# Kernel optimization log

Measured on AMD Instinct MI355X. Metric: run time of the kernel, lower is better.

Reference implementation:

```python
import jax, jax.numpy as jnp
import numpy as np

B, S, D = 4, 2048, 512
QKD = 256
HID = 3 * D  # expansion_factor=3
EPS = 1e-5


def _ln(x, g, b):
    m = jnp.mean(x, axis=-1, keepdims=True)
    v = jnp.mean((x - m) ** 2, axis=-1, keepdims=True)
    return (x - m) * jax.lax.rsqrt(v + EPS) * g + b


def setup_inputs() -> dict:
    key = jax.random.key(0)
    ks = jax.random.split(key, 12)
    s = lambda fan: 1.0 / np.sqrt(fan)
    return {
        "x":  jax.random.normal(ks[0], (B, S, D), jnp.float32),
        "Wm": jax.random.uniform(ks[1], (D, D), jnp.float32, -s(D), s(D)),
        "bm": jnp.zeros((D,), jnp.float32),
        "g1": jnp.ones((D,), jnp.float32),
        "b1": jnp.zeros((D,), jnp.float32),
        "Wh": jax.random.uniform(ks[2], (2 * HID, D), jnp.float32, -s(D), s(D)),
        "bh": jnp.zeros((2 * HID,), jnp.float32),
        "Wq": jax.random.uniform(ks[3], (QKD, D), jnp.float32, -s(D), s(D)),
        "bq": jnp.zeros((QKD,), jnp.float32),
        "Wb": jax.random.normal(ks[4], (QKD, QKD), jnp.float32),
        "Wo": jax.random.uniform(ks[5], (D, HID), jnp.float32, -s(HID), s(HID)),
        "bo": jnp.zeros((D,), jnp.float32),
        "g2": jnp.ones((D,), jnp.float32),
        "b2": jnp.zeros((D,), jnp.float32),
    }


def reference(x, Wm, bm, g1, b1, Wh, bh, Wq, bq, Wb, Wo, bo, g2, b2):
    seq_len = x.shape[-2]
    memory = jnp.einsum('bsd,ed->bse', x, Wm) + bm
    normed = _ln(x + memory, g1, b1)
    h = jax.nn.relu(jnp.einsum('bsd,hd->bsh', normed, Wh) + bh)
    v, gate = h[..., :HID], h[..., HID:]
    Z = jax.nn.relu(jnp.einsum('bsd,qd->bsq', normed, Wq) + bq)  # [B,S,QKD]
    QK = jnp.einsum('bid,de,bje->bij', Z, Wb, Z) / seq_len
    A = jax.nn.relu(QK) ** 2  # relu^2 attention, no softmax
    V = jnp.einsum('bij,bjd->bid', A, v) * gate
    out = _ln(jnp.einsum('bsh,dh->bsd', V, Wo) + bo, g2, b2)
    return out + x
```

## Files before the change

kernel.cpp:

```cpp
#include <hip/hip_runtime.h>

typedef unsigned short u16;
typedef unsigned char u8;
typedef __attribute__((ext_vector_type(8))) short short8;
typedef __attribute__((ext_vector_type(4))) float f32x4;
typedef __attribute__((ext_vector_type(8))) int int8v;
typedef __attribute__((ext_vector_type(4))) int int4v;

#define LN_EPS 1e-5f
#define SCALE_A 4096.f
#define SCALE_V 8.f
#define INV_SCALE_AV (1.f/32768.f)
#define SCALE_NRM 4.f
#define SCALE_WH 512.f
#define INV_SCALE_H (1.f/2048.f)
#define MX_ONE 0x7F7F7F7Fu

__device__ __forceinline__ u16 f2bf(float f){
    union { float f; unsigned u; } c; c.f = f;
    unsigned u = c.u + 0x7FFFu + ((c.u >> 16) & 1u);
    return (u16)(u >> 16);
}
__device__ __forceinline__ float bf2f(u16 h){
    union { unsigned u; float f; } c; c.u = ((unsigned)h) << 16;
    return c.f;
}
__device__ __forceinline__ u8 f2fp8(float f){
    int r = __builtin_amdgcn_cvt_pk_fp8_f32(f, 0.f, 0, false);
    return (u8)(r & 0xFF);
}
__device__ __forceinline__ u16 f2fp8x2(float a, float b){
    int r = __builtin_amdgcn_cvt_pk_fp8_f32(a, b, 0, false);
    return (u16)(r & 0xFFFF);
}

enum { EPI_NONE=0, EPI_BIAS_RES, EPI_BIAS_RELU, EPI_RELUSQ };
enum { OT_F32=0, OT_BF16=1, OT_FP8=2 };

__device__ __forceinline__ void gl2lds16(const void* g, void* lds){
    __builtin_amdgcn_global_load_lds(
        (const __attribute__((address_space(1))) unsigned*)g,
        (__attribute__((address_space(3))) unsigned*)lds, 16, 0, 0);
}

template<int EPI, int OT>
__device__ __forceinline__ void bf16_gemm_body(
    u16* sA, u16* sB,
    const u16* Az, const u16* Bz, void* Cv,
    int K, int lda, int ldb, int ldc, size_t zc,
    int m0, int n0,
    const float* bias, const float* ext, int ldext, float scale)
{
    const int tid = threadIdx.x;
    const int lane = tid & 63, quad = lane >> 4, l15 = lane & 15;
    const int wave = tid >> 6;
    const int wm = (wave >> 1) * 64, wn = (wave & 1) * 64;

    const u16* gA[2]; const u16* gB[2]; int lo[2];
#pragma unroll
    for (int r = 0; r < 2; r++){
        const int c = tid + r * 256;
        gA[r] = Az + (size_t)(m0 + (c & 127)) * lda + (c >> 7) * 8;
        gB[r] = Bz + (size_t)(n0 + (c & 127)) * ldb + (c >> 7) * 8;
        lo[r] = ((tid & 192) + r * 256) * 16;
    }

    f32x4 acc[4][4];
#pragma unroll
    for (int i = 0; i < 4; i++)
#pragma unroll
        for (int j = 0; j < 4; j++) acc[i][j] = (f32x4){0.f,0.f,0.f,0.f};

    const u16* fA = sA + quad * 1024 + (wm + l15) * 8;
    const u16* fB = sB + quad * 1024 + (wn + l15) * 8;

    for (int k0 = 0; k0 < K; k0 += 32){
#pragma unroll
        for (int r = 0; r < 2; r++){
            gl2lds16(gA[r] + k0, (char*)sA + lo[r]);
            gl2lds16(gB[r] + k0, (char*)sB + lo[r]);
        }
        __syncthreads();
        short8 a[4], b[4];
#pragma unroll
        for (int t = 0; t < 4; t++){
            a[t] = *(const short8*)(fA + t * 128);
            b[t] = *(const short8*)(fB + t * 128);
        }
#pragma unroll
        for (int i = 0; i < 4; i++)
#pragma unroll
            for (int j = 0; j < 4; j++)
                acc[i][j] = __builtin_amdgcn_mfma_f32_16x16x32_bf16(a[i], b[j], acc[i][j], 0, 0, 0);
        __syncthreads();
    }

    float* Cf = (float*)Cv; u16* Ch = (u16*)Cv; u8* C8 = (u8*)Cv;
#pragma unroll
    for (int i = 0; i < 4; i++){
#pragma unroll
        for (int j = 0; j < 4; j++){
            const int n = n0 + wn + j * 16 + l15;
            float bs = (EPI==EPI_BIAS_RES || EPI==EPI_BIAS_RELU) ? bias[n] : 0.f;
#pragma unroll
            for (int r = 0; r < 4; r++){
                const int m = m0 + wm + i * 16 + quad * 4 + r;
                float v = acc[i][j][r] + bs;
                if (EPI==EPI_BIAS_RES) v += ext[(size_t)m * ldext + n];
                if (EPI==EPI_BIAS_RELU) v = fmaxf(v, 0.f);
                if (EPI==EPI_RELUSQ){ float t = fmaxf(v * scale, 0.f); v = t * t * SCALE_A; }
                if (OT==OT_FP8)       C8[zc + (size_t)m * ldc + n] = f2fp8(v);
                else if (OT==OT_BF16) Ch[zc + (size_t)m * ldc + n] = f2bf(v);
                else                  Cf[zc + (size_t)m * ldc + n] = v;
            }
        }
    }
}

template<int EPI, int OT>
__global__ __launch_bounds__(256)
void mgemm(const u16* __restrict__ A, const u16* __restrict__ B, void* __restrict__ Cv,
           int K, int lda, int ldb, int ldc,
           long sAb, long sBb, long sCb,
           const float* __restrict__ bias,
           const float* __restrict__ ext, int ldext,
           float scale)
{
    __shared__ u16 sA[4096];
    __shared__ u16 sB[4096];
    const int z = blockIdx.z;
    bf16_gemm_body<EPI,OT>(sA, sB,
        A + (size_t)z * sAb, B + (size_t)z * sBb, Cv,
        K, lda, ldb, ldc, (size_t)z * sCb,
        blockIdx.y * 128, blockIdx.x * 128,
        bias, ext, ldext, scale);
}

template<bool VOUT>
__device__ __forceinline__ void mx_gemm_body(
    u8* sA, u8* sB,
    const u8* Az, const u8* Bz, u16* C,
    int K, int lda, int ldb, int ldc, size_t zc,
    int m0, int n0,
    const u16* gate, int ldext, size_t ze,
    const float* bias, u8* vout)
{
    const int tid = threadIdx.x;
    const int lane = tid & 63, quad = lane >> 4, l15 = lane & 15;
    const int wave = tid >> 6;
    const int wm = (wave >> 1) * 64, wn = (wave & 1) * 64;

    const u8* gA[4]; const u8* gB[4]; int lo[4];
#pragma unroll
    for (int p = 0; p < 4; p++){
        const int r = p * 32 + (tid >> 3);
        const int j = (tid & 7) ^ (r & 7);
        gA[p] = Az + (size_t)(m0 + r) * lda + j * 16;
        gB[p] = Bz + (size_t)(n0 + r) * ldb + j * 16;
        lo[p] = p * 4096 + wave * 1024;
    }

    f32x4 acc[4][4];
#pragma unroll
    for (int i = 0; i < 4; i++)
#pragma unroll
        for (int j = 0; j < 4; j++) acc[i][j] = (f32x4){0.f,0.f,0.f,0.f};

    for (int k0 = 0; k0 < K; k0 += 128){
#pragma unroll
        for (int p = 0; p < 4; p++){
            gl2lds16(gA[p] + k0, (char*)sA + lo[p]);
            gl2lds16(gB[p] + k0, (char*)sB + lo[p]);
        }
        __syncthreads();
        int8v a[4], b[4];
#pragma unroll
        for (int i = 0; i < 4; i++){
            const int m = wm + i * 16 + l15;
            const int4v a0 = *(const int4v*)(sA + m * 128 + ((2*quad    ) ^ (m & 7)) * 16);
            const int4v a1 = *(const int4v*)(sA + m * 128 + ((2*quad + 1) ^ (m & 7)) * 16);
            a[i] = (int8v){a0[0],a0[1],a0[2],a0[3],a1[0],a1[1],a1[2],a1[3]};
            const int n = wn + i * 16 + l15;
            const int4v b0 = *(const int4v*)(sB + n * 128 + ((2*quad    ) ^ (n & 7)) * 16);
            const int4v b1 = *(const int4v*)(sB + n * 128 + ((2*quad + 1) ^ (n & 7)) * 16);
            b[i] = (int8v){b0[0],b0[1],b0[2],b0[3],b1[0],b1[1],b1[2],b1[3]};
        }
#pragma unroll
        for (int i = 0; i < 4; i++)
#pragma unroll
            for (int j = 0; j < 4; j++)
                acc[i][j] = __builtin_amdgcn_mfma_scale_f32_16x16x128_f8f6f4(
                    a[i], b[j], acc[i][j], 0, 0, 0, MX_ONE, 0, MX_ONE);
        __syncthreads();
    }

#pragma unroll
    for (int i = 0; i < 4; i++){
#pragma unroll
        for (int j = 0; j < 4; j++){
            const int n = n0 + wn + j * 16 + l15;
#pragma unroll
            for (int r = 0; r < 4; r++){
                const int m = m0 + wm + i * 16 + quad * 4 + r;
                if (VOUT){
                    float h = fmaxf(acc[i][j][r] * INV_SCALE_H + bias[n], 0.f);
                    vout[(size_t)m * 1536 + n] = f2fp8(h * SCALE_V);
                } else {
                    float v = acc[i][j][r] * INV_SCALE_AV
                            * bf2f(gate[ze + (size_t)m * ldext + n]);
                    C[zc + (size_t)m * ldc + n] = f2bf(v);
                }
            }
        }
    }
}

__global__ __launch_bounds__(256)
void mgemm8mx(const u8* __restrict__ A, const u8* __restrict__ B, u16* __restrict__ C,
              int K, int lda, int ldb, int ldc,
              long sAb, long sBb, long sCb,
              const u16* __restrict__ gate, int ldext, long sEb)
{
    __shared__ u8 sA[16384];
    __shared__ u8 sB[16384];
    const int z = blockIdx.z;
    mx_gemm_body<false>(sA, sB,
        A + (size_t)z * sAb, B + (size_t)z * sBb, C,
        K, lda, ldb, ldc, (size_t)z * sCb,
        blockIdx.y * 128, blockIdx.x * 128,
        gate, ldext, (size_t)z * sEb, nullptr, nullptr);
}

__global__ __launch_bounds__(256)
void dual3_k(const u16* __restrict__ nrm, const u16* __restrict__ n8,
             const u8* __restrict__ Wh8, const u16* __restrict__ Whgb,
             const u16* __restrict__ Wqbf,
             const float* __restrict__ bh, const float* __restrict__ bq,
             u8* __restrict__ v8, u16* __restrict__ gbf, u16* __restrict__ Zb)
{
    __shared__ char lds[32768];
    const int bx = blockIdx.x;
    const int m0 = blockIdx.y * 128;
    if (bx < 12){
        mx_gemm_body<true>((u8*)lds, (u8*)lds + 16384,
            (const u8*)n8, Wh8, nullptr,
            512, 512, 512, 0, 0,
            m0, bx * 128,
            nullptr, 0, 0, bh, v8);
    } else if (bx < 24){
        bf16_gemm_body<EPI_BIAS_RELU,OT_BF16>((u16*)lds, (u16*)lds + 4096,
            nrm, Whgb, gbf,
            512, 512, 512, 1536, 0,
            m0, (bx - 12) * 128,
            bh + 1536, nullptr, 0, 1.f);
    } else {
        bf16_gemm_body<EPI_BIAS_RELU,OT_BF16>((u16*)lds, (u16*)lds + 4096,
            nrm, Wqbf, Zb,
            512, 512, 512, 256, 0,
            m0, (bx - 24) * 128,
            bq, nullptr, 0, 1.f);
    }
}

__global__ __launch_bounds__(256)
void batch6_k(const u16* __restrict__ ZWbb, const u16* __restrict__ Zb,
              u8* __restrict__ A8,
              const u8* __restrict__ v8, u8* __restrict__ vT8)
{
    __shared__ char lds[16384];
    const int bx = blockIdx.x;
    const int z  = blockIdx.y;
    const int S = 2048, QKD = 256, HID = 1536;
    if (bx < 256){
        bf16_gemm_body<EPI_RELUSQ,OT_FP8>((u16*)lds, (u16*)lds + 4096,
            ZWbb + (size_t)z * S * QKD, Zb + (size_t)z * S * QKD, A8,
            QKD, QKD, QKD, S, (size_t)z * S * S,
            (bx >> 4) * 128, (bx & 15) * 128,
            nullptr, nullptr, 0, 1.f/(float)S);
    } else {
        const int idx = bx - 256;
        const int h0 = (idx % 24) * 64, s0 = (idx / 24) * 64;
        u8 (*t)[68] = (u8(*)[68])lds;
        const u8* vb = v8 + (size_t)z * S * HID;
        u8* vTb = vT8 + (size_t)z * HID * S;
        const int tid = threadIdx.x;
#pragma unroll
        for (int i = 0; i < 4; i++){
            int id2 = tid + i * 256;
            int r = id2 >> 4, c4 = (id2 & 15) * 4;
            uchar4 u = *(const uchar4*)(vb + (size_t)(s0 + r) * HID + h0 + c4);
            t[r][c4] = u.x; t[r][c4+1] = u.y; t[r][c4+2] = u.z; t[r][c4+3] = u.w;
        }
        __syncthreads();
#pragma unroll
        for (int i = 0; i < 4; i++){
            int id2 = tid + i * 256;
            int r = id2 >> 4, c4 = (id2 & 15) * 4;
            uchar4 u;
            u.x = t[c4][r]; u.y = t[c4+1][r]; u.z = t[c4+2][r]; u.w = t[c4+3][r];
            *(uchar4*)(vTb + (size_t)(h0 + r) * S + s0 + c4) = u;
        }
    }
}

__global__ __launch_bounds__(256)
void ln1_k(const float* __restrict__ in, const float* __restrict__ g,
           const float* __restrict__ b, u16* __restrict__ nbf, u16* __restrict__ n8)
{
    const int row = blockIdx.x, tid = threadIdx.x;
    const size_t base = (size_t)row * 512 + tid * 2;
    const float2 v = *(const float2*)(in + base);
    float s = v.x + v.y, ss = v.x * v.x + v.y * v.y;
#pragma unroll
    for (int off = 32; off > 0; off >>= 1){
        s  += __shfl_down(s,  off);
        ss += __shfl_down(ss, off);
    }
    __shared__ float sbuf[8], ssbuf[8];
    const int wid = tid >> 6, lane = tid & 63;
    if (lane == 0){ sbuf[wid] = s; ssbuf[wid] = ss; }
    __syncthreads();
    if (tid == 0){
        float S = 0.f, SS = 0.f;
#pragma unroll
        for (int i = 0; i < 4; i++){ S += sbuf[i]; SS += ssbuf[i]; }
        const float mean = S * (1.f/512.f);
        const float var  = SS * (1.f/512.f) - mean * mean;
        sbuf[4]  = mean;
        ssbuf[4] = rsqrtf(var + LN_EPS);
    }
    __syncthreads();
    const float mean = sbuf[4], rstd = ssbuf[4];
    const float2 gg = *(const float2*)(g + tid * 2);
    const float2 bb = *(const float2*)(b + tid * 2);
    const float ox = (v.x - mean) * rstd * gg.x + bb.x;
    const float oy = (v.y - mean) * rstd * gg.y + bb.y;
    ((unsigned*)nbf)[(size_t)row * 256 + tid] =
        ((unsigned)f2bf(oy) << 16) | (unsigned)f2bf(ox);
    n8[(size_t)row * 256 + tid] = f2fp8x2(ox * SCALE_NRM, oy * SCALE_NRM);
}

__global__ __launch_bounds__(256)
void ln2_k(const u16* __restrict__ pa, long pstride,
           const float* __restrict__ bias2,
           const float* __restrict__ g, const float* __restrict__ b,
           const float* __restrict__ x, float* __restrict__ out)
{
    const int row = blockIdx.x, tid = threadIdx.x;
    const size_t base = (size_t)row * 512 + tid * 2;
    const unsigned p0 = ((const unsigned*)pa)[(size_t)row * 256 + tid];
    const unsigned p1 = ((const unsigned*)(pa + pstride))[(size_t)row * 256 + tid];
    const float2 bb2 = *(const float2*)(bias2 + tid * 2);
    float2 v;
    v.x = bf2f((u16)p0) + bf2f((u16)p1) + bb2.x;
    v.y = bf2f((u16)(p0 >> 16)) + bf2f((u16)(p1 >> 16)) + bb2.y;
    float s = v.x + v.y, ss = v.x * v.x + v.y * v.y;
#pragma unroll
    for (int off = 32; off > 0; off >>= 1){
        s  += __shfl_down(s,  off);
        ss += __shfl_down(ss, off);
    }
    __shared__ float sbuf[8], ssbuf[8];
    const int wid = tid >> 6, lane = tid & 63;
    if (lane == 0){ sbuf[wid] = s; ssbuf[wid] = ss; }
    __syncthreads();
    if (tid == 0){
        float S = 0.f, SS = 0.f;
#pragma unroll
        for (int i = 0; i < 4; i++){ S += sbuf[i]; SS += ssbuf[i]; }
        const float mean = S * (1.f/512.f);
        const float var  = SS * (1.f/512.f) - mean * mean;
        sbuf[4]  = mean;
        ssbuf[4] = rsqrtf(var + LN_EPS);
    }
    __syncthreads();
    const float mean = sbuf[4], rstd = ssbuf[4];
    const float2 gg = *(const float2*)(g + tid * 2);
    const float2 bb = *(const float2*)(b + tid * 2);
    const float2 r = *(const float2*)(x + base);
    float2 o;
    o.x = (v.x - mean) * rstd * gg.x + bb.x + r.x;
    o.y = (v.y - mean) * rstd * gg.y + bb.y + r.y;
    *(float2*)(out + base) = o;
}

__global__ __launch_bounds__(256)
void castall_k(const float* __restrict__ x, const float* __restrict__ Wm,
               const float* __restrict__ Wh, const float* __restrict__ Wq,
               const float* __restrict__ Wo, const float* __restrict__ Wb,
               u16* __restrict__ xb, u16* __restrict__ Wmb, u8* __restrict__ Wh8,
               u16* __restrict__ Whgb,
               u16* __restrict__ Wqb, u16* __restrict__ Wob, u16* __restrict__ WbT)
{
    const int i = blockIdx.x * 256 + threadIdx.x;
    if (i >= 1736704){
        const int j = i - 1736704;
        if (j < 65536){
            const int e = j >> 8, d = j & 255;
            WbT[e * 256 + d] = f2bf(Wb[d * 256 + e]);
        }
        return;
    }
    if (i >= 1114112 && i < 1310720){
        const int off = i - 1114112;
        const float4 v = ((const float4*)Wh)[off];
        unsigned r0 = (unsigned)f2fp8x2(v.x * SCALE_WH, v.y * SCALE_WH);
        unsigned r1 = (unsigned)f2fp8x2(v.z * SCALE_WH, v.w * SCALE_WH);
        ((unsigned*)Wh8)[off] = r0 | (r1 << 16);
        return;
    }
    const float* src; u16* dst; int off;
    if      (i < 1048576){ src = x;  dst = xb;   off = i; }
    else if (i < 1114112){ src = Wm; dst = Wmb;  off = i - 1048576; }
    else if (i < 1507328){ src = Wh + 786432; dst = Whgb; off = i - 1310720; }
    else if (i < 1540096){ src = Wq; dst = Wqb;  off = i - 1507328; }
    else                 { src = Wo; dst = Wob;  off = i - 1540096; }
    const float4 v = ((const float4*)src)[off];
    ushort4 o; o.x = f2bf(v.x); o.y = f2bf(v.y); o.z = f2bf(v.z); o.w = f2bf(v.w);
    ((ushort4*)dst)[off] = o;
}

extern "C" void kernel_launch(void* const* d_in, const int* in_sizes, int n_in,
                              void* d_out, int out_size, void* d_ws, size_t ws_size,
                              hipStream_t stream)
{
    const float* x  = (const float*)d_in[0];
    const float* Wm = (const float*)d_in[1];
    const float* bm = (const float*)d_in[2];
    const float* g1 = (const float*)d_in[3];
    const float* b1 = (const float*)d_in[4];
    const float* Wh = (const float*)d_in[5];
    const float* bh = (const float*)d_in[6];
    const float* Wq = (const float*)d_in[7];
    const float* bq = (const float*)d_in[8];
    const float* Wb = (const float*)d_in[9];
    const float* Wo = (const float*)d_in[10];
    const float* bo = (const float*)d_in[11];
    const float* g2 = (const float*)d_in[12];
    const float* b2 = (const float*)d_in[13];
    float* out = (float*)d_out;
    (void)in_sizes; (void)n_in; (void)out_size; (void)ws_size;

    const int Bn=4, S=2048, D=512, QKD=256, HID=1536;
    const int M = Bn * S;
    const long MD = (long)M * D;

    char* p = (char*)d_ws;
    auto alloc = [&](size_t bytes)->void*{ void* r = p; p += (bytes + 255) & ~(size_t)255; return r; };
    u16*  xbf  = (u16*) alloc((size_t)M*D*2);
    u16*  Wmbf = (u16*) alloc((size_t)D*D*2);
    u8*   Wh8  = (u8*)  alloc((size_t)HID*D);
    u16*  Whgb = (u16*) alloc((size_t)HID*D*2);
    u16*  Wqbf = (u16*) alloc((size_t)QKD*D*2);
    u16*  Wobf = (u16*) alloc((size_t)D*HID*2);
    u16*  WbT  = (u16*) alloc((size_t)QKD*QKD*2);
    float* ybuf= (float*)alloc((size_t)MD*4);
    u16*  wop  = (u16*) alloc((size_t)MD*2*2);
    u16*  n8   = (u16*) alloc((size_t)M*D);
    u16*  Zb   = (u16*) alloc((size_t)M*QKD*2);
    u16*  ZWbb = (u16*) alloc((size_t)M*QKD*2);
    u8*   v8   = (u8*)  alloc((size_t)M*HID);
    u16*  gbf  = (u16*) alloc((size_t)M*HID*2);
    u8*   vT8  = (u8*)  alloc((size_t)M*HID);
    u8*   A8   = (u8*)  alloc((size_t)M*S);
    u16*  Vgbf = (u16*) alloc((size_t)M*HID*2);
    u16*  nrm  = xbf;

    dim3 blk(256);

    castall_k<<<dim3(7040), blk, 0, stream>>>(x, Wm, Wh, Wq, Wo, Wb,
                                              xbf, Wmbf, Wh8, Whgb, Wqbf, Wobf, WbT);
    mgemm<EPI_BIAS_RES,OT_F32><<<dim3(D/128, M/128, 1), blk, 0, stream>>>(
        xbf, Wmbf, ybuf, D, D, D, D, 0,0,0, bm, x, D, 1.f);
    ln1_k<<<dim3(M), blk, 0, stream>>>(ybuf, g1, b1, nrm, n8);
    dual3_k<<<dim3(26, M/128), blk, 0, stream>>>(
        nrm, n8, Wh8, Whgb, Wqbf, bh, bq, v8, gbf, Zb);
    mgemm<EPI_NONE,OT_BF16><<<dim3(QKD/128, M/128, 1), blk, 0, stream>>>(
        Zb, WbT, ZWbb, QKD, QKD, QKD, QKD, 0,0,0, nullptr, nullptr, 0, 1.f);
    batch6_k<<<dim3(1024, Bn), blk, 0, stream>>>(ZWbb, Zb, A8, v8, vT8);
    mgemm8mx<<<dim3(HID/128, S/128, Bn), blk, 0, stream>>>(
        A8, vT8, Vgbf, S, S, S, HID,
        (long)S*S, (long)HID*S, (long)S*HID,
        gbf, HID, (long)S*HID);
    mgemm<EPI_NONE,OT_BF16><<<dim3(D/128, M/128, 2), blk, 0, stream>>>(
        Vgbf, Wobf, wop, HID/2, HID, HID, D, 768, 768, MD,
        nullptr, nullptr, 0, 1.f);
    ln2_k<<<dim3(M), blk, 0, stream>>>(wop, MD, bo, g2, b2, x, out);
}
```

Before: 321.1 us.

## Fuse all stages into one persistent cooperative kernel with grid syncs

Replaces the nine separate kernel launches with a single cooperative persistent kernel. Each stage becomes a grid-stride loop over tiles or rows, and grid.sync() separates the stages. This removes per-launch overhead and the tail idle time between launches. In exchange it caps occupancy through a fixed grid size and launch bounds, gives every stage the larger 32KB LDS footprint, and adds grid-wide barrier cost and possible load imbalance.

```diff
diff --git a/kernel.cpp b/kernel.cpp
--- a/kernel.cpp
+++ b/kernel.cpp
@@ -1,4 +1,7 @@
 #include <hip/hip_runtime.h>
+#include <hip/hip_cooperative_groups.h>
+
+namespace cg = cooperative_groups;
 
 typedef unsigned short u16;
 typedef unsigned char u8;
@@ -115,25 +118,6 @@
             }
         }
     }
-}
-
-template<int EPI, int OT>
-__global__ __launch_bounds__(256)
-void mgemm(const u16* __restrict__ A, const u16* __restrict__ B, void* __restrict__ Cv,
-           int K, int lda, int ldb, int ldc,
-           long sAb, long sBb, long sCb,
-           const float* __restrict__ bias,
-           const float* __restrict__ ext, int ldext,
-           float scale)
-{
-    __shared__ u16 sA[4096];
-    __shared__ u16 sB[4096];
-    const int z = blockIdx.z;
-    bf16_gemm_body<EPI,OT>(sA, sB,
-        A + (size_t)z * sAb, B + (size_t)z * sBb, Cv,
-        K, lda, ldb, ldc, (size_t)z * sCb,
-        blockIdx.y * 128, blockIdx.x * 128,
-        bias, ext, ldext, scale);
 }
 
 template<bool VOUT>
@@ -215,235 +199,227 @@
     }
 }
 
-__global__ __launch_bounds__(256)
-void mgemm8mx(const u8* __restrict__ A, const u8* __restrict__ B, u16* __restrict__ C,
-              int K, int lda, int ldb, int ldc,
-              long sAb, long sBb, long sCb,
-              const u16* __restrict__ gate, int ldext, long sEb)
-{
-    __shared__ u8 sA[16384];
-    __shared__ u8 sB[16384];
-    const int z = blockIdx.z;
-    mx_gemm_body<false>(sA, sB,
-        A + (size_t)z * sAb, B + (size_t)z * sBb, C,
-        K, lda, ldb, ldc, (size_t)z * sCb,
-        blockIdx.y * 128, blockIdx.x * 128,
-        gate, ldext, (size_t)z * sEb, nullptr, nullptr);
-}
-
-__global__ __launch_bounds__(256)
-void dual3_k(const u16* __restrict__ nrm, const u16* __restrict__ n8,
-             const u8* __restrict__ Wh8, const u16* __restrict__ Whgb,
-             const u16* __restrict__ Wqbf,
-             const float* __restrict__ bh, const float* __restrict__ bq,
-             u8* __restrict__ v8, u16* __restrict__ gbf, u16* __restrict__ Zb)
-{
-    __shared__ char lds[32768];
-    const int bx = blockIdx.x;
-    const int m0 = blockIdx.y * 128;
-    if (bx < 12){
-        mx_gemm_body<true>((u8*)lds, (u8*)lds + 16384,
-            (const u8*)n8, Wh8, nullptr,
-            512, 512, 512, 0, 0,
-            m0, bx * 128,
-            nullptr, 0, 0, bh, v8);
-    } else if (bx < 24){
-        bf16_gemm_body<EPI_BIAS_RELU,OT_BF16>((u16*)lds, (u16*)lds + 4096,
-            nrm, Whgb, gbf,
-            512, 512, 512, 1536, 0,
-            m0, (bx - 12) * 128,
-            bh + 1536, nullptr, 0, 1.f);
-    } else {
-        bf16_gemm_body<EPI_BIAS_RELU,OT_BF16>((u16*)lds, (u16*)lds + 4096,
-            nrm, Wqbf, Zb,
-            512, 512, 512, 256, 0,
-            m0, (bx - 24) * 128,
-            bq, nullptr, 0, 1.f);
-    }
-}
-
-__global__ __launch_bounds__(256)
-void batch6_k(const u16* __restrict__ ZWbb, const u16* __restrict__ Zb,
-              u8* __restrict__ A8,
-              const u8* __restrict__ v8, u8* __restrict__ vT8)
-{
-    __shared__ char lds[16384];
-    const int bx = blockIdx.x;
-    const int z  = blockIdx.y;
-    const int S = 2048, QKD = 256, HID = 1536;
-    if (bx < 256){
-        bf16_gemm_body<EPI_RELUSQ,OT_FP8>((u16*)lds, (u16*)lds + 4096,
-            ZWbb + (size_t)z * S * QKD, Zb + (size_t)z * S * QKD, A8,
-            QKD, QKD, QKD, S, (size_t)z * S * S,
-            (bx >> 4) * 128, (bx & 15) * 128,
-            nullptr, nullptr, 0, 1.f/(float)S);
-    } else {
-        const int idx = bx - 256;
-        const int h0 = (idx % 24) * 64, s0 = (idx / 24) * 64;
-        u8 (*t)[68] = (u8(*)[68])lds;
-        const u8* vb = v8 + (size_t)z * S * HID;
-        u8* vTb = vT8 + (size_t)z * HID * S;
-        const int tid = threadIdx.x;
-#pragma unroll
-        for (int i = 0; i < 4; i++){
-            int id2 = tid + i * 256;
-            int r = id2 >> 4, c4 = (id2 & 15) * 4;
-            uchar4 u = *(const uchar4*)(vb + (size_t)(s0 + r) * HID + h0 + c4);
-            t[r][c4] = u.x; t[r][c4+1] = u.y; t[r][c4+2] = u.z; t[r][c4+3] = u.w;
-        }
-        __syncthreads();
-#pragma unroll
-        for (int i = 0; i < 4; i++){
-            int id2 = tid + i * 256;
-            int r = id2 >> 4, c4 = (id2 & 15) * 4;
-            uchar4 u;
-            u.x = t[c4][r]; u.y = t[c4+1][r]; u.z = t[c4+2][r]; u.w = t[c4+3][r];
-            *(uchar4*)(vTb + (size_t)(h0 + r) * S + s0 + c4) = u;
-        }
-    }
-}
-
-__global__ __launch_bounds__(256)
-void ln1_k(const float* __restrict__ in, const float* __restrict__ g,
-           const float* __restrict__ b, u16* __restrict__ nbf, u16* __restrict__ n8)
-{
-    const int row = blockIdx.x, tid = threadIdx.x;
-    const size_t base = (size_t)row * 512 + tid * 2;
-    const float2 v = *(const float2*)(in + base);
-    float s = v.x + v.y, ss = v.x * v.x + v.y * v.y;
-#pragma unroll
-    for (int off = 32; off > 0; off >>= 1){
-        s  += __shfl_down(s,  off);
-        ss += __shfl_down(ss, off);
-    }
-    __shared__ float sbuf[8], ssbuf[8];
-    const int wid = tid >> 6, lane = tid & 63;
-    if (lane == 0){ sbuf[wid] = s; ssbuf[wid] = ss; }
-    __syncthreads();
-    if (tid == 0){
-        float S = 0.f, SS = 0.f;
-#pragma unroll
-        for (int i = 0; i < 4; i++){ S += sbuf[i]; SS += ssbuf[i]; }
-        const float mean = S * (1.f/512.f);
-        const float var  = SS * (1.f/512.f) - mean * mean;
-        sbuf[4]  = mean;
-        ssbuf[4] = rsqrtf(var + LN_EPS);
-    }
-    __syncthreads();
-    const float mean = sbuf[4], rstd = ssbuf[4];
-    const float2 gg = *(const float2*)(g + tid * 2);
-    const float2 bb = *(const float2*)(b + tid * 2);
-    const float ox = (v.x - mean) * rstd * gg.x + bb.x;
-    const float oy = (v.y - mean) * rstd * gg.y + bb.y;
-    ((unsigned*)nbf)[(size_t)row * 256 + tid] =
-        ((unsigned)f2bf(oy) << 16) | (unsigned)f2bf(ox);
-    n8[(size_t)row * 256 + tid] = f2fp8x2(ox * SCALE_NRM, oy * SCALE_NRM);
-}
-
-__global__ __launch_bounds__(256)
-void ln2_k(const u16* __restrict__ pa, long pstride,
-           const float* __restrict__ bias2,
-           const float* __restrict__ g, const float* __restrict__ b,
-           const float* __restrict__ x, float* __restrict__ out)
-{
-    const int row = blockIdx.x, tid = threadIdx.x;
-    const size_t base = (size_t)row * 512 + tid * 2;
-    const unsigned p0 = ((const unsigned*)pa)[(size_t)row * 256 + tid];
-    const unsigned p1 = ((const unsigned*)(pa + pstride))[(size_t)row * 256 + tid];
-    const float2 bb2 = *(const float2*)(bias2 + tid * 2);
-    float2 v;
-    v.x = bf2f((u16)p0) + bf2f((u16)p1) + bb2.x;
-    v.y = bf2f((u16)(p0 >> 16)) + bf2f((u16)(p1 >> 16)) + bb2.y;
-    float s = v.x + v.y, ss = v.x * v.x + v.y * v.y;
-#pragma unroll
-    for (int off = 32; off > 0; off >>= 1){
-        s  += __shfl_down(s,  off);
-        ss += __shfl_down(ss, off);
-    }
-    __shared__ float sbuf[8], ssbuf[8];
-    const int wid = tid >> 6, lane = tid & 63;
-    if (lane == 0){ sbuf[wid] = s; ssbuf[wid] = ss; }
-    __syncthreads();
-    if (tid == 0){
-        float S = 0.f, SS = 0.f;
-#pragma unroll
-        for (int i = 0; i < 4; i++){ S += sbuf[i]; SS += ssbuf[i]; }
-        const float mean = S * (1.f/512.f);
-        const float var  = SS * (1.f/512.f) - mean * mean;
-        sbuf[4]  = mean;
-        ssbuf[4] = rsqrtf(var + LN_EPS);
-    }
-    __syncthreads();
-    const float mean = sbuf[4], rstd = ssbuf[4];
-    const float2 gg = *(const float2*)(g + tid * 2);
-    const float2 bb = *(const float2*)(b + tid * 2);
-    const float2 r = *(const float2*)(x + base);
-    float2 o;
-    o.x = (v.x - mean) * rstd * gg.x + bb.x + r.x;
-    o.y = (v.y - mean) * rstd * gg.y + bb.y + r.y;
-    *(float2*)(out + base) = o;
-}
-
-__global__ __launch_bounds__(256)
-void castall_k(const float* __restrict__ x, const float* __restrict__ Wm,
-               const float* __restrict__ Wh, const float* __restrict__ Wq,
-               const float* __restrict__ Wo, const float* __restrict__ Wb,
-               u16* __restrict__ xb, u16* __restrict__ Wmb, u8* __restrict__ Wh8,
-               u16* __restrict__ Whgb,
-               u16* __restrict__ Wqb, u16* __restrict__ Wob, u16* __restrict__ WbT)
-{
-    const int i = blockIdx.x * 256 + threadIdx.x;
+struct MegaArgs {
+    const float *x, *Wm, *bm, *g1, *b1, *Wh, *bh, *Wq, *bq, *Wb, *Wo, *bo, *g2, *b2;
+    float* out;
+    u16 *xbf, *Wmbf; u8* Wh8; u16 *Whgb, *Wqbf, *Wobf, *WbT;
+    float* ybuf; u16* wop; u16* n8; u16 *Zb, *ZWbb;
+    u8* v8; u16* gbf; u8 *vT8, *A8; u16* Vgbf;
+};
+
+__device__ __forceinline__ void cast_item(int i, const MegaArgs& a){
     if (i >= 1736704){
         const int j = i - 1736704;
         if (j < 65536){
             const int e = j >> 8, d = j & 255;
-            WbT[e * 256 + d] = f2bf(Wb[d * 256 + e]);
+            a.WbT[e * 256 + d] = f2bf(a.Wb[d * 256 + e]);
         }
         return;
     }
     if (i >= 1114112 && i < 1310720){
         const int off = i - 1114112;
-        const float4 v = ((const float4*)Wh)[off];
+        const float4 v = ((const float4*)a.Wh)[off];
         unsigned r0 = (unsigned)f2fp8x2(v.x * SCALE_WH, v.y * SCALE_WH);
         unsigned r1 = (unsigned)f2fp8x2(v.z * SCALE_WH, v.w * SCALE_WH);
-        ((unsigned*)Wh8)[off] = r0 | (r1 << 16);
+        ((unsigned*)a.Wh8)[off] = r0 | (r1 << 16);
         return;
     }
     const float* src; u16* dst; int off;
-    if      (i < 1048576){ src = x;  dst = xb;   off = i; }
-    else if (i < 1114112){ src = Wm; dst = Wmb;  off = i - 1048576; }
-    else if (i < 1507328){ src = Wh + 786432; dst = Whgb; off = i - 1310720; }
-    else if (i < 1540096){ src = Wq; dst = Wqb;  off = i - 1507328; }
-    else                 { src = Wo; dst = Wob;  off = i - 1540096; }
+    if      (i < 1048576){ src = a.x;  dst = a.xbf;   off = i; }
+    else if (i < 1114112){ src = a.Wm; dst = a.Wmbf;  off = i - 1048576; }
+    else if (i < 1507328){ src = a.Wh + 786432; dst = a.Whgb; off = i - 1310720; }
+    else if (i < 1540096){ src = a.Wq; dst = a.Wqbf;  off = i - 1507328; }
+    else                 { src = a.Wo; dst = a.Wobf;  off = i - 1540096; }
     const float4 v = ((const float4*)src)[off];
     ushort4 o; o.x = f2bf(v.x); o.y = f2bf(v.y); o.z = f2bf(v.z); o.w = f2bf(v.w);
     ((ushort4*)dst)[off] = o;
+}
+
+__device__ __forceinline__ void tr8_item(int z, int idx, const MegaArgs& a, char* lds){
+    const int S = 2048, HID = 1536;
+    const int h0 = (idx % 24) * 64, s0 = (idx / 24) * 64;
+    u8 (*t)[68] = (u8(*)[68])lds;
+    const u8* vb = a.v8 + (size_t)z * S * HID;
+    u8* vTb = a.vT8 + (size_t)z * HID * S;
+    const int tid = threadIdx.x;
+#pragma unroll
+    for (int i = 0; i < 4; i++){
+        int id2 = tid + i * 256;
+        int r = id2 >> 4, c4 = (id2 & 15) * 4;
+        uchar4 u = *(const uchar4*)(vb + (size_t)(s0 + r) * HID + h0 + c4);
+        t[r][c4] = u.x; t[r][c4+1] = u.y; t[r][c4+2] = u.z; t[r][c4+3] = u.w;
+    }
+    __syncthreads();
+#pragma unroll
+    for (int i = 0; i < 4; i++){
+        int id2 = tid + i * 256;
+        int r = id2 >> 4, c4 = (id2 & 15) * 4;
+        uchar4 u;
+        u.x = t[c4][r]; u.y = t[c4+1][r]; u.z = t[c4+2][r]; u.w = t[c4+3][r];
+        *(uchar4*)(vTb + (size_t)(h0 + r) * S + s0 + c4) = u;
+    }
+    __syncthreads();
+}
+
+__device__ __forceinline__ void ln_reduce(float2 v, float* sred, float& mean, float& rstd){
+    const int tid = threadIdx.x;
+    float s = v.x + v.y, ss = v.x * v.x + v.y * v.y;
+#pragma unroll
+    for (int off = 32; off > 0; off >>= 1){
+        s  += __shfl_down(s,  off);
+        ss += __shfl_down(ss, off);
+    }
+    float* sbuf = sred; float* ssbuf = sred + 8;
+    const int wid = tid >> 6, lane = tid & 63;
+    if (lane == 0){ sbuf[wid] = s; ssbuf[wid] = ss; }
+    __syncthreads();
+    if (tid == 0){
+        float S = 0.f, SS = 0.f;
+#pragma unroll
+        for (int i = 0; i < 4; i++){ S += sbuf[i]; SS += ssbuf[i]; }
+        const float m = S * (1.f/512.f);
+        const float var = SS * (1.f/512.f) - m * m;
+        sbuf[4]  = m;
+        ssbuf[4] = rsqrtf(var + LN_EPS);
+    }
+    __syncthreads();
+    mean = sbuf[4]; rstd = ssbuf[4];
+}
+
+__device__ __forceinline__ void ln1_row(int row, const MegaArgs& a, float* sred){
+    const int tid = threadIdx.x;
+    __syncthreads();
+    const size_t base = (size_t)row * 512 + tid * 2;
+    const float2 v = *(const float2*)(a.ybuf + base);
+    float mean, rstd;
+    ln_reduce(v, sred, mean, rstd);
+    const float2 gg = *(const float2*)(a.g1 + tid * 2);
+    const float2 bb = *(const float2*)(a.b1 + tid * 2);
+    const float ox = (v.x - mean) * rstd * gg.x + bb.x;
+    const float oy = (v.y - mean) * rstd * gg.y + bb.y;
+    ((unsigned*)a.xbf)[(size_t)row * 256 + tid] =
+        ((unsigned)f2bf(oy) << 16) | (unsigned)f2bf(ox);
+    a.n8[(size_t)row * 256 + tid] = f2fp8x2(ox * SCALE_NRM, oy * SCALE_NRM);
+}
+
+__device__ __forceinline__ void ln2_row(int row, const MegaArgs& a, float* sred){
+    const int tid = threadIdx.x;
+    __syncthreads();
+    const long MD = 4194304;
+    const size_t base = (size_t)row * 512 + tid * 2;
+    const unsigned p0 = ((const unsigned*)a.wop)[(size_t)row * 256 + tid];
+    const unsigned p1 = ((const unsigned*)(a.wop + MD))[(size_t)row * 256 + tid];
+    const float2 bb2 = *(const float2*)(a.bo + tid * 2);
+    float2 v;
+    v.x = bf2f((u16)p0) + bf2f((u16)p1) + bb2.x;
+    v.y = bf2f((u16)(p0 >> 16)) + bf2f((u16)(p1 >> 16)) + bb2.y;
+    float mean, rstd;
+    ln_reduce(v, sred, mean, rstd);
+    const float2 gg = *(const float2*)(a.g2 + tid * 2);
+    const float2 bb = *(const float2*)(a.b2 + tid * 2);
+    const float2 r = *(const float2*)(a.x + base);
+    float2 o;
+    o.x = (v.x - mean) * rstd * gg.x + bb.x + r.x;
+    o.y = (v.y - mean) * rstd * gg.y + bb.y + r.y;
+    *(float2*)(a.out + base) = o;
+}
+
+__global__ __launch_bounds__(256, 4)
+void mega_k(MegaArgs a)
+{
+    __shared__ char lds[32768];
+    cg::grid_group grid = cg::this_grid();
+    const int G = gridDim.x;
+    const int bid = blockIdx.x;
+    const int tid = threadIdx.x;
+    u16* s16 = (u16*)lds;
+    u8*  s8  = (u8*)lds;
+    float* sred = (float*)lds;
+    const int S = 2048, QKD = 256, HID = 1536;
+    const long MD = 4194304;
+
+    for (int i = bid * 256 + tid; i < 1802240; i += G * 256) cast_item(i, a);
+    grid.sync();
+
+    for (int t = bid; t < 256; t += G)
+        bf16_gemm_body<EPI_BIAS_RES,OT_F32>(s16, s16 + 4096,
+            a.xbf, a.Wmbf, a.ybuf, 512, 512, 512, 512, 0,
+            (t >> 2) * 128, (t & 3) * 128, a.bm, a.x, 512, 1.f);
+    grid.sync();
+
+    for (int r = bid; r < 8192; r += G) ln1_row(r, a, sred);
+    grid.sync();
+
+    for (int t = bid; t < 1664; t += G){
+        const int bx = t % 26, m0 = (t / 26) * 128;
+        if (bx < 12){
+            mx_gemm_body<true>(s8, s8 + 16384,
+                (const u8*)a.n8, a.Wh8, nullptr,
+                512, 512, 512, 0, 0, m0, bx * 128,
+                nullptr, 0, 0, a.bh, a.v8);
+        } else if (bx < 24){
+            bf16_gemm_body<EPI_BIAS_RELU,OT_BF16>(s16, s16 + 4096,
+                a.xbf, a.Whgb, a.gbf, 512, 512, 512, 1536, 0,
+                m0, (bx - 12) * 128, a.bh + 1536, nullptr, 0, 1.f);
+        } else {
+            bf16_gemm_body<EPI_BIAS_RELU,OT_BF16>(s16, s16 + 4096,
+                a.xbf, a.Wqbf, a.Zb, 512, 512, 512, 256, 0,
+                m0, (bx - 24) * 128, a.bq, nullptr, 0, 1.f);
+        }
+    }
+    grid.sync();
+
+    for (int t = bid; t < 128; t += G)
+        bf16_gemm_body<EPI_NONE,OT_BF16>(s16, s16 + 4096,
+            a.Zb, a.WbT, a.ZWbb, 256, 256, 256, 256, 0,
+            (t >> 1) * 128, (t & 1) * 128, nullptr, nullptr, 0, 1.f);
+    grid.sync();
+
+    for (int t = bid; t < 4096; t += G){
+        const int z = t >> 10, bx = t & 1023;
+        if (bx < 256){
+            bf16_gemm_body<EPI_RELUSQ,OT_FP8>(s16, s16 + 4096,
+                a.ZWbb + (size_t)z * S * QKD, a.Zb + (size_t)z * S * QKD, a.A8,
+                QKD, QKD, QKD, S, (size_t)z * S * S,
+                (bx >> 4) * 128, (bx & 15) * 128,
+                nullptr, nullptr, 0, 1.f / (float)S);
+        } else {
+            tr8_item(z, bx - 256, a, lds);
+        }
+    }
+    grid.sync();
+
+    for (int t = bid; t < 768; t += G){
+        const int z = t / 192, rem = t % 192;
+        const int bx = rem % 12, by = rem / 12;
+        mx_gemm_body<false>(s8, s8 + 16384,
+            a.A8 + (size_t)z * S * S, a.vT8 + (size_t)z * HID * S, a.Vgbf,
+            S, S, S, HID, (size_t)z * S * HID,
+            by * 128, bx * 128,
+            a.gbf, HID, (size_t)z * S * HID, nullptr, nullptr);
+    }
+    grid.sync();
+
+    for (int t = bid; t < 512; t += G){
+        const int z = t >> 8, rem = t & 255;
+        bf16_gemm_body<EPI_NONE,OT_BF16>(s16, s16 + 4096,
+            a.Vgbf + (size_t)z * 768, a.Wobf + (size_t)z * 768, a.wop,
+            768, 1536, 1536, 512, (size_t)z * MD,
+            (rem >> 2) * 128, (rem & 3) * 128, nullptr, nullptr, 0, 1.f);
+    }
+    grid.sync();
+
+    for (int r = bid; r < 8192; r += G) ln2_row(r, a, sred);
 }
 
 extern "C" void kernel_launch(void* const* d_in, const int* in_sizes, int n_in,
                               void* d_out, int out_size, void* d_ws, size_t ws_size,
                               hipStream_t stream)
 {
-    const float* x  = (const float*)d_in[0];
-    const float* Wm = (const float*)d_in[1];
-    const float* bm = (const float*)d_in[2];
-    const float* g1 = (const float*)d_in[3];
-    const float* b1 = (const float*)d_in[4];
-    const float* Wh = (const float*)d_in[5];
-    const float* bh = (const float*)d_in[6];
-    const float* Wq = (const float*)d_in[7];
-    const float* bq = (const float*)d_in[8];
-    const float* Wb = (const float*)d_in[9];
-    const float* Wo = (const float*)d_in[10];
-    const float* bo = (const float*)d_in[11];
-    const float* g2 = (const float*)d_in[12];
-    const float* b2 = (const float*)d_in[13];
-    float* out = (float*)d_out;
-    (void)in_sizes; (void)n_in; (void)out_size; (void)ws_size;
-
     const int Bn=4, S=2048, D=512, QKD=256, HID=1536;
     const int M = Bn * S;
     const long MD = (long)M * D;
+    (void)in_sizes; (void)n_in; (void)out_size; (void)ws_size;
 
     char* p = (char*)d_ws;
     auto alloc = [&](size_t bytes)->void*{ void* r = p; p += (bytes + 255) & ~(size_t)255; return r; };
@@ -464,26 +440,27 @@
     u8*   vT8  = (u8*)  alloc((size_t)M*HID);
     u8*   A8   = (u8*)  alloc((size_t)M*S);
     u16*  Vgbf = (u16*) alloc((size_t)M*HID*2);
-    u16*  nrm  = xbf;
-
-    dim3 blk(256);
-
-    castall_k<<<dim3(7040), blk, 0, stream>>>(x, Wm, Wh, Wq, Wo, Wb,
-                                              xbf, Wmbf, Wh8, Whgb, Wqbf, Wobf, WbT);
-    mgemm<EPI_BIAS_RES,OT_F32><<<dim3(D/128, M/128, 1), blk, 0, stream>>>(
-        xbf, Wmbf, ybuf, D, D, D, D, 0,0,0, bm, x, D, 1.f);
-    ln1_k<<<dim3(M), blk, 0, stream>>>(ybuf, g1, b1, nrm, n8);
-    dual3_k<<<dim3(26, M/128), blk, 0, stream>>>(
-        nrm, n8, Wh8, Whgb, Wqbf, bh, bq, v8, gbf, Zb);
-    mgemm<EPI_NONE,OT_BF16><<<dim3(QKD/128, M/128, 1), blk, 0, stream>>>(
-        Zb, WbT, ZWbb, QKD, QKD, QKD, QKD, 0,0,0, nullptr, nullptr, 0, 1.f);
-    batch6_k<<<dim3(1024, Bn), blk, 0, stream>>>(ZWbb, Zb, A8, v8, vT8);
-    mgemm8mx<<<dim3(HID/128, S/128, Bn), blk, 0, stream>>>(
-        A8, vT8, Vgbf, S, S, S, HID,
-        (long)S*S, (long)HID*S, (long)S*HID,
-        gbf, HID, (long)S*HID);
-    mgemm<EPI_NONE,OT_BF16><<<dim3(D/128, M/128, 2), blk, 0, stream>>>(
-        Vgbf, Wobf, wop, HID/2, HID, HID, D, 768, 768, MD,
-        nullptr, nullptr, 0, 1.f);
-    ln2_k<<<dim3(M), blk, 0, stream>>>(wop, MD, bo, g2, b2, x, out);
-}
+
+    MegaArgs a;
+    a.x  = (const float*)d_in[0];  a.Wm = (const float*)d_in[1];
+    a.bm = (const float*)d_in[2];  a.g1 = (const float*)d_in[3];
+    a.b1 = (const float*)d_in[4];  a.Wh = (const float*)d_in[5];
+    a.bh = (const float*)d_in[6];  a.Wq = (const float*)d_in[7];
+    a.bq = (const float*)d_in[8];  a.Wb = (const float*)d_in[9];
+    a.Wo = (const float*)d_in[10]; a.bo = (const float*)d_in[11];
+    a.g2 = (const float*)d_in[12]; a.b2 = (const float*)d_in[13];
+    a.out = (float*)d_out;
+    a.xbf = xbf; a.Wmbf = Wmbf; a.Wh8 = Wh8; a.Whgb = Whgb;
+    a.Wqbf = Wqbf; a.Wobf = Wobf; a.WbT = WbT;
+    a.ybuf = ybuf; a.wop = wop; a.n8 = n8; a.Zb = Zb; a.ZWbb = ZWbb;
+    a.v8 = v8; a.gbf = gbf; a.vT8 = vT8; a.A8 = A8; a.Vgbf = Vgbf;
+
+    int maxB = 0;
+    hipOccupancyMaxActiveBlocksPerMultiprocessor(&maxB, mega_k, 256, 0);
+    int G = maxB * 256;
+    if (G <= 0)   G = 768;
+    if (G > 2048) G = 2048;
+
+    void* params[] = { (void*)&a };
+    hipLaunchCooperativeKernel(mega_k, dim3(G), dim3(256), params, 0, stream);
+}
```

Measured after the change: 1.052 ms. 3.28x slower.
